# Optimization experiments

Measured on AMD Instinct MI355X. Metric: run time of the kernel, lower is better.

The kernel has to match this reference:

```python
import jax, jax.numpy as jnp
import numpy as np

N = 100000   # nodes
E = 1600000  # edges (node pairs)
D = 64       # msg_feature_len
H = 128      # hidden width of gate/message MLPs


def setup_inputs() -> dict:
    key = jax.random.key(0)
    ks = jax.random.split(key, 10)
    s = 0.05
    return {
        "node_weights": jax.random.uniform(ks[0], (N, 1), dtype=jnp.float32),
        "node_prev_features": jax.random.normal(ks[1], (N, D), dtype=jnp.float32),
        "self_idx": jax.random.randint(ks[2], (E,), 0, N),
        "neighbor_idx": jax.random.randint(ks[3], (E,), 0, N),
        "gw1": jax.random.normal(ks[4], (2 * D, H), dtype=jnp.float32) * s,
        "gb1": jnp.zeros((H,), jnp.float32),
        "gw2": jax.random.normal(ks[5], (H, 1), dtype=jnp.float32) * s,
        "gb2": jnp.zeros((1,), jnp.float32),
        "mw1": jax.random.normal(ks[6], (2 * D, H), dtype=jnp.float32) * s,
        "mb1": jnp.zeros((H,), jnp.float32),
        "mw2": jax.random.normal(ks[7], (H, D), dtype=jnp.float32) * s,
        "mb2": jnp.zeros((D,), jnp.float32),
        "pow_p": jax.random.normal(ks[8], (1,), dtype=jnp.float32),
    }


def reference(node_weights, node_prev_features, self_idx, neighbor_idx,
              gw1, gb1, gw2, gb2, mw1, mb1, mw2, mb2, pow_p):
    # gather + concat: message [E, 2D]
    msg = jnp.concatenate(
        [node_prev_features[self_idx], node_prev_features[neighbor_idx]], axis=1)
    w = node_weights[neighbor_idx]  # [E, 1]

    # gate MLP (Linear -> ReLU -> Linear): [E, 1]
    gate = jax.nn.relu(msg @ gw1 + gb1) @ gw2 + gb2
    # segment-softmax over edges grouped by self_idx, weighted by w**pow
    gmax = jax.ops.segment_max(gate, self_idx, num_segments=N)  # [N, 1]
    gate = (w ** pow_p) * jnp.exp(gate - gmax[self_idx])
    gsum = jax.ops.segment_sum(gate, self_idx, num_segments=N)  # [N, 1]
    gate = gate / (gsum[self_idx] + 1e-10)

    # message MLP: [E, D]
    x = jax.nn.relu(msg @ mw1 + mb1) @ mw2 + mb2

    # weighted scatter-sum back to nodes; single head -> mean is identity
    node_update = jax.ops.segment_sum(gate * x, self_idx, num_segments=N)
    return node_update + node_prev_features
```

## Files before the change

### kernel.cpp

```cpp
#include <hip/hip_runtime.h>
#include <hip/hip_bf16.h>

typedef __bf16 bf16x8 __attribute__((ext_vector_type(8)));
typedef float f32x4 __attribute__((ext_vector_type(4)));
typedef float f32x2 __attribute__((ext_vector_type(2)));

#define WIN 64
#define TILE 112
#define CHUNK 7
#define HSTR 136
#define SCAN_BLK 1024
#define SENT 0x7f7f7f7f

static __device__ __forceinline__ void dec8(unsigned x, unsigned y, float* o) {
    f32x2 a = __builtin_amdgcn_cvt_pk_f32_fp8(x, false);
    f32x2 b = __builtin_amdgcn_cvt_pk_f32_fp8(x, true);
    f32x2 c = __builtin_amdgcn_cvt_pk_f32_fp8(y, false);
    f32x2 d = __builtin_amdgcn_cvt_pk_f32_fp8(y, true);
    o[0] = a[0]; o[1] = a[1]; o[2] = b[0]; o[3] = b[1];
    o[4] = c[0]; o[5] = c[1]; o[6] = d[0]; o[7] = d[1];
}

__global__ void k_wconv(const float* __restrict__ gw1, const float* __restrict__ mw1,
                        const float* __restrict__ mw2,
                        __bf16* __restrict__ Bt, __bf16* __restrict__ mw2t,
                        int* __restrict__ hist, int* __restrict__ s_lo,
                        int* __restrict__ s_hi, int N, int NB)
{
    int i = blockIdx.x * 256 + threadIdx.x;
    if (i < 32768) {
        int c = i >> 6, k = i & 63;
        float v;
        if (c < 128)      v = gw1[k * 128 + c];
        else if (c < 256) v = gw1[(64 + k) * 128 + (c - 128)];
        else if (c < 384) v = mw1[k * 128 + (c - 256)];
        else              v = mw1[(64 + k) * 128 + (c - 384)];
        Bt[i] = (__bf16)v;
    } else if (i < 40960) {
        int j = i - 32768;
        int c = j >> 7, k = j & 127;
        mw2t[j] = (__bf16)mw2[k * 64 + c];
    }
    if (i < N) hist[i] = 0;
    if (i < NB) { s_lo[i] = SENT; s_hi[i] = 0; }
}

__global__ void __launch_bounds__(256, 4)
k_tab(const float* __restrict__ feat, const __bf16* __restrict__ Bt,
      const float* __restrict__ gb1, const float* __restrict__ mb1,
      const int* __restrict__ selfi, int* __restrict__ hist,
      unsigned char* __restrict__ Tp, unsigned char* __restrict__ Tq, int N, int E)
{
    __shared__ unsigned char ldsT[2][16][256];

    for (int e = blockIdx.x * 256 + threadIdx.x; e < E; e += gridDim.x * 256)
        atomicAdd(&hist[selfi[e]], 1);

    const int tid = threadIdx.x;
    const int lane = tid & 63, wv = tid >> 6;
    const int la = lane & 15, kg = lane >> 4;
    const int r0 = blockIdx.x * 16;
    if (r0 >= N) return;

    bf16x8 a[2];
    #pragma unroll
    for (int kk = 0; kk < 2; ++kk) {
        const int rr = min(r0 + la, N - 1);
        const float* src = feat + (size_t)rr * 64 + kk * 32 + kg * 8;
        f32x4 f0 = *reinterpret_cast<const f32x4*>(src);
        f32x4 f1 = *reinterpret_cast<const f32x4*>(src + 4);
        #pragma unroll
        for (int j = 0; j < 4; ++j) { a[kk][j] = (__bf16)f0[j]; a[kk][4 + j] = (__bf16)f1[j]; }
    }
    #pragma unroll
    for (int j = 0; j < 8; ++j) {
        const int c = wv * 128 + j * 16 + la;
        float bias = 0.f;
        if (c < 128) bias = gb1[c];
        else if (c >= 256 && c < 384) bias = mb1[c - 256];
        f32x4 acc = {bias, bias, bias, bias};
        #pragma unroll
        for (int kk = 0; kk < 2; ++kk) {
            bf16x8 bb = *reinterpret_cast<const bf16x8*>(Bt + (size_t)c * 64 + kk * 32 + kg * 8);
            acc = __builtin_amdgcn_mfma_f32_16x16x32_bf16(a[kk], bb, acc, 0, 0, 0);
        }
        int tbl, boff;
        if (c < 128)      { tbl = 0; boff = ((c) >> 3) * 16 + (c & 7); }
        else if (c < 256) { const int q = c - 128; tbl = 1; boff = (q >> 3) * 16 + (q & 7); }
        else if (c < 384) { const int q = c - 256; tbl = 0; boff = (q >> 3) * 16 + 8 + (q & 7); }
        else              { const int q = c - 384; tbl = 1; boff = (q >> 3) * 16 + 8 + (q & 7); }
        #pragma unroll
        for (int i = 0; i < 4; ++i) {
            const int pk = __builtin_amdgcn_cvt_pk_fp8_f32(acc[i], acc[i], 0, false);
            ldsT[tbl][kg * 4 + i][boff] = (unsigned char)(pk & 0xff);
        }
    }
    __syncthreads();
    {
        const int row = tid >> 4, v4 = tid & 15;
        if (r0 + row < N) {
            const uint4* s0p = reinterpret_cast<const uint4*>(&ldsT[0][row][0]);
            const uint4* s1p = reinterpret_cast<const uint4*>(&ldsT[1][row][0]);
            reinterpret_cast<uint4*>(Tp + (size_t)(r0 + row) * 256)[v4] = s0p[v4];
            reinterpret_cast<uint4*>(Tq + (size_t)(r0 + row) * 256)[v4] = s1p[v4];
        }
    }
}

__global__ void k_scan1(const int* __restrict__ hist, int* __restrict__ incl,
                        int* __restrict__ bsum, int N)
{
    __shared__ int sd[SCAN_BLK];
    int i = blockIdx.x * SCAN_BLK + threadIdx.x;
    int v = (i < N) ? hist[i] : 0;
    sd[threadIdx.x] = v;
    __syncthreads();
    for (int off = 1; off < SCAN_BLK; off <<= 1) {
        int t = (threadIdx.x >= off) ? sd[threadIdx.x - off] : 0;
        __syncthreads();
        sd[threadIdx.x] += t;
        __syncthreads();
    }
    if (i < N) incl[i] = sd[threadIdx.x];
    if (threadIdx.x == SCAN_BLK - 1) bsum[blockIdx.x] = sd[SCAN_BLK - 1];
}

__global__ void k_scan23(const int* __restrict__ incl, const int* __restrict__ hist,
                         const int* __restrict__ bsum,
                         int* __restrict__ cursor, int* __restrict__ starts,
                         int* __restrict__ s_lo, int* __restrict__ s_hi,
                         float* __restrict__ lpw, const float* __restrict__ nodew,
                         const float* __restrict__ powp,
                         const float* __restrict__ prev, float* __restrict__ out,
                         int N, int E)
{
    __shared__ int boff_s;
    if (threadIdx.x < 64) {
        int part = 0;
        for (int j = threadIdx.x; j < (int)blockIdx.x; j += 64) part += bsum[j];
        #pragma unroll
        for (int sh = 1; sh < 64; sh <<= 1) part += __shfl_xor(part, sh, 64);
        if (threadIdx.x == 0) boff_s = part;
    }
    __syncthreads();
    int i = blockIdx.x * SCAN_BLK + threadIdx.x;
    if (i >= N) return;
    const int h = hist[i];
    const int v = incl[i] - h + boff_s;
    cursor[i] = v;
    starts[i] = v;
    lpw[i] = powp[0] * __logf(nodew[i]);
    if (h > 0) {
        const int b = v / WIN;
        atomicMin(&s_lo[b], i);
        atomicMax(&s_hi[b], i + 1);
    } else {
        const float* ps = prev + (size_t)i * 64;
        float* po = out + (size_t)i * 64;
        for (int k = 0; k < 64; ++k) po[k] = ps[k];
    }
}

__global__ void k_scatter(const int* __restrict__ selfi, const int* __restrict__ nbri,
                          int* __restrict__ cursor, int* __restrict__ nbr_p, int E)
{
    int e = blockIdx.x * 256 + threadIdx.x;
    if (e >= E) return;
    int s = selfi[e];
    int pos = atomicAdd(&cursor[s], 1);
    nbr_p[pos] = nbri[e];
}

__global__ void __launch_bounds__(256, 5)
k_fused(const unsigned char* __restrict__ Tp, const unsigned char* __restrict__ Tq,
        const int* __restrict__ nbr_p, const int* __restrict__ starts,
        const int* __restrict__ s_lo, const int* __restrict__ s_hi,
        const float* __restrict__ lpw,
        const float* __restrict__ gw2, const float* __restrict__ gb2,
        const __bf16* __restrict__ mw2t, const float* __restrict__ mb2,
        const float* __restrict__ prev, float* __restrict__ out,
        int N, int E)
{
    __shared__ __align__(16) unsigned char hlds8[TILE][HSTR];
    __shared__ float logit_s[TILE];
    __shared__ float ginv_s[WIN];
    __shared__ int st_s[WIN + 1];

    const int b = blockIdx.x;
    const int s0 = s_lo[b];
    if (s0 == SENT) return;
    const int s1 = s_hi[b];
    const int nseg = s1 - s0;
    const int e0 = starts[s0];
    const int e1 = (s1 < N) ? starts[s1] : E;
    int ne = e1 - e0;
    if (ne > TILE) ne = TILE;

    const int tid = threadIdx.x;
    for (int j = tid; j <= nseg; j += 256)
        st_s[j] = (j < nseg) ? starts[s0 + j] : e1;
    __syncthreads();

    const int lane = tid & 63, wv = tid >> 6;
    const int g16 = tid >> 4, il = tid & 15;

    {
        const float b2v = gb2[0];
        float w2f[8];
        {
            f32x4 wa = *reinterpret_cast<const f32x4*>(gw2 + il * 8);
            f32x4 wb = *reinterpret_cast<const f32x4*>(gw2 + il * 8 + 4);
            w2f[0] = wa[0]; w2f[1] = wa[1]; w2f[2] = wa[2]; w2f[3] = wa[3];
            w2f[4] = wb[0]; w2f[5] = wb[1]; w2f[6] = wb[2]; w2f[7] = wb[3];
        }
        const int ck = (ne + 15) >> 4;
        const int rb = g16 * ck;
        const int re = min(rb + ck, ne);
        const int m = re - rb;
        if (m > 0) {
            uint4 qv[CHUNK];
            float lpv[CHUNK];
            #pragma unroll
            for (int j = 0; j < CHUNK; ++j) {
                const int rc = (j < m) ? (rb + j) : (re - 1);
                const int nn = nbr_p[e0 + rc];
                qv[j] = *reinterpret_cast<const uint4*>(Tq + (size_t)nn * 256 + il * 16);
                lpv[j] = lpw[nn];
            }
            int cur;
            {
                int lo = 0, hi = nseg - 1;
                while (lo < hi) {
                    const int mid = (lo + hi + 1) >> 1;
                    if (st_s[mid] <= e0 + rb) lo = mid; else hi = mid - 1;
                }
                cur = lo;
            }
            int curlim = st_s[cur + 1];
            float pgf[8], pmf[8];
            {
                const uint4 tpv = *reinterpret_cast<const uint4*>(Tp + (size_t)(s0 + cur) * 256 + il * 16);
                dec8(tpv.x, tpv.y, pgf);
                dec8(tpv.z, tpv.w, pmf);
            }
            #pragma unroll
            for (int j = 0; j < CHUNK; ++j) {
                if (j < m) {
                    const int r = rb + j;
                    if (e0 + r >= curlim) {
                        do { ++cur; curlim = st_s[cur + 1]; } while (e0 + r >= curlim);
                        const uint4 tpv = *reinterpret_cast<const uint4*>(Tp + (size_t)(s0 + cur) * 256 + il * 16);
                        dec8(tpv.x, tpv.y, pgf);
                        dec8(tpv.z, tpv.w, pmf);
                    }
                    float qgv[8], qmv[8];
                    dec8(qv[j].x, qv[j].y, qgv);
                    dec8(qv[j].z, qv[j].w, qmv);
                    float lg = 0.f;
                    float hm[8];
                    #pragma unroll
                    for (int q = 0; q < 8; ++q) {
                        lg = fmaf(fmaxf(pgf[q] + qgv[q], 0.f), w2f[q], lg);
                        hm[q] = fmaxf(pmf[q] + qmv[q], 0.f);
                    }
                    unsigned d0 = __builtin_amdgcn_cvt_pk_fp8_f32(hm[0], hm[1], 0, false);
                    d0 = __builtin_amdgcn_cvt_pk_fp8_f32(hm[2], hm[3], d0, true);
                    unsigned d1 = __builtin_amdgcn_cvt_pk_fp8_f32(hm[4], hm[5], 0, false);
                    d1 = __builtin_amdgcn_cvt_pk_fp8_f32(hm[6], hm[7], d1, true);
                    *reinterpret_cast<uint2*>(&hlds8[r][il * 8]) = make_uint2(d0, d1);
                    #pragma unroll
                    for (int sh = 1; sh < 16; sh <<= 1)
                        lg += __shfl_xor(lg, sh, 16);
                    if (il == 0) logit_s[r] = lg + b2v + lpv[j];
                }
            }
        }
    }
    __syncthreads();

    const int la = lane & 15, kg = lane >> 4;
    const int row0[2] = {wv * 16, 64 + wv * 16};
    const bool lv[2] = {row0[0] < ne, (wv < 3) && (row0[1] < ne)};

    f32x4 c2[2][4] = {};
    #pragma unroll
    for (int kk = 0; kk < 4; ++kk) {
        const int kboff = kk * 32 + kg * 8;
        bf16x8 a[2];
        #pragma unroll
        for (int m2 = 0; m2 < 2; ++m2)
            if (lv[m2]) {
                const uint2 hw = *reinterpret_cast<const uint2*>(&hlds8[row0[m2] + la][kboff]);
                float t[8];
                dec8(hw.x, hw.y, t);
                #pragma unroll
                for (int q = 0; q < 8; ++q) a[m2][q] = (__bf16)t[q];
            }
        #pragma unroll
        for (int n = 0; n < 4; ++n) {
            bf16x8 bb = *reinterpret_cast<const bf16x8*>(mw2t + (size_t)(n * 16 + la) * 128 + kboff);
            #pragma unroll
            for (int m2 = 0; m2 < 2; ++m2)
                if (lv[m2]) c2[m2][n] = __builtin_amdgcn_mfma_f32_16x16x32_bf16(a[m2], bb, c2[m2][n], 0, 0, 0);
        }
    }

    for (int j = g16; j < nseg; j += 16) {
        int a0 = st_s[j] - e0;
        int a1 = st_s[j + 1] - e0;
        if (a1 > ne) a1 = ne;
        float mx = -3.4e38f;
        for (int idx = a0 + il; idx < a1; idx += 16)
            mx = fmaxf(mx, logit_s[idx]);
        #pragma unroll
        for (int sh = 1; sh < 16; sh <<= 1)
            mx = fmaxf(mx, __shfl_xor(mx, sh, 16));
        float sum = 0.f;
        for (int idx = a0 + il; idx < a1; idx += 16) {
            const float g = __expf(logit_s[idx] - mx);
            logit_s[idx] = g;
            sum += g;
        }
        #pragma unroll
        for (int sh = 1; sh < 16; sh <<= 1)
            sum += __shfl_xor(sum, sh, 16);
        if (il == 0) ginv_s[j] = 1.f / (sum + 1e-10f);
    }
    __syncthreads();

    __bf16 (*xb)[68] = reinterpret_cast<__bf16(*)[68]>(&hlds8[0][0]);
    #pragma unroll
    for (int m2 = 0; m2 < 2; ++m2) {
        if (!lv[m2]) continue;
        #pragma unroll
        for (int n = 0; n < 4; ++n) {
            const float b2v = mb2[n * 16 + la];
            #pragma unroll
            for (int i = 0; i < 4; ++i) {
                const int row = row0[m2] + kg * 4 + i;
                const float v = (row < ne) ? logit_s[row] * (c2[m2][n][i] + b2v) : 0.f;
                xb[row][n * 16 + la] = (__bf16)v;
            }
        }
    }
    __syncthreads();

    for (int j = wv; j < nseg; j += 4) {
        int a0 = st_s[j] - e0;
        int a1 = st_s[j + 1] - e0;
        if (a1 > ne) a1 = ne;
        if (a1 <= a0) continue;
        float sum = 0.f;
        for (int r = a0; r < a1; ++r) sum += (float)xb[r][lane];
        const float gi = ginv_s[j];
        const size_t o = (size_t)(s0 + j) * 64 + lane;
        out[o] = prev[o] + sum * gi;
    }
}

extern "C" void kernel_launch(void* const* d_in, const int* in_sizes, int n_in,
                              void* d_out, int out_size, void* d_ws, size_t ws_size,
                              hipStream_t stream)
{
    const float* node_w = (const float*)d_in[0];
    const float* prev   = (const float*)d_in[1];
    const int*   selfi  = (const int*)d_in[2];
    const int*   nbri   = (const int*)d_in[3];
    const float* gw1 = (const float*)d_in[4];
    const float* gb1 = (const float*)d_in[5];
    const float* gw2 = (const float*)d_in[6];
    const float* gb2 = (const float*)d_in[7];
    const float* mw1 = (const float*)d_in[8];
    const float* mb1 = (const float*)d_in[9];
    const float* mw2 = (const float*)d_in[10];
    const float* mb2 = (const float*)d_in[11];
    const float* powp = (const float*)d_in[12];
    const int N = in_sizes[0];
    const int E = in_sizes[2];
    float* out = (float*)d_out;
    const int NB = (E + WIN - 1) / WIN;

    char* ws = (char*)d_ws;
    size_t off = 0;
    auto alloc = [&](size_t bytes) {
        void* p = ws + off;
        off = (off + bytes + 255) & ~(size_t)255;
        return p;
    };
    unsigned char* Tp    = (unsigned char*)alloc((size_t)N * 256);
    unsigned char* Tq    = (unsigned char*)alloc((size_t)N * 256);
    __bf16* Bt           = (__bf16*)alloc(512 * 64 * 2);
    __bf16* mw2t         = (__bf16*)alloc(64 * 128 * 2);
    int* nbr_p           = (int*)alloc((size_t)E * 4);
    int* hist            = (int*)alloc((size_t)N * 4);
    int* cursor          = (int*)alloc((size_t)N * 4);
    int* starts          = (int*)alloc((size_t)N * 4);
    int* incl            = (int*)alloc((size_t)N * 4);
    float* lpw           = (float*)alloc((size_t)N * 4);
    int* s_lo            = (int*)alloc((size_t)NB * 4);
    int* s_hi            = (int*)alloc((size_t)NB * 4);
    const int nb = (N + SCAN_BLK - 1) / SCAN_BLK;
    int* bsum            = (int*)alloc((size_t)nb * 4);

    int initN = N;
    if (initN < 40960) initN = 40960;
    if (initN < NB) initN = NB;
    k_wconv<<<(initN + 255) / 256, 256, 0, stream>>>(gw1, mw1, mw2, Bt, mw2t,
                                                     hist, s_lo, s_hi, N, NB);
    k_tab<<<(N + 15) / 16, 256, 0, stream>>>(prev, Bt, gb1, mb1, selfi, hist, Tp, Tq, N, E);
    k_scan1<<<nb, SCAN_BLK, 0, stream>>>(hist, incl, bsum, N);
    k_scan23<<<nb, SCAN_BLK, 0, stream>>>(incl, hist, bsum, cursor, starts, s_lo, s_hi,
                                          lpw, node_w, powp, prev, out, N, E);
    k_scatter<<<(E + 255) / 256, 256, 0, stream>>>(selfi, nbri, cursor, nbr_p, E);
    k_fused<<<NB, 256, 0, stream>>>(Tp, Tq, nbr_p, starts, s_lo, s_hi, lpw,
                                    gw2, gb2, mw2t, mb2, prev, out, N, E);
}
```

Baseline: 503.1 us.

## Stage fused-kernel hidden activations in bf16 and use shuffle-based block scan

Hidden message-MLP activations are stored in LDS as bf16 instead of fp8, and the weighted outputs as fp32 instead of bf16. This removes the fp8 encode/decode and bf16 conversions around the second MFMA and the segment reduction, at the cost of doubled LDS footprint and traffic. The block prefix scan now uses wave shuffles instead of a barrier-heavy Hillis-Steele loop. Buffer initialization moves from the weight-conversion kernel to hipMemsetAsync calls, which adds launches.

```diff
diff --git a/kernel.cpp b/kernel.cpp
--- a/kernel.cpp
+++ b/kernel.cpp
@@ -8,7 +8,7 @@
 #define WIN 64
 #define TILE 112
 #define CHUNK 7
-#define HSTR 136
+#define LSTR 136
 #define SCAN_BLK 1024
 #define SENT 0x7f7f7f7f
 
@@ -23,9 +23,7 @@
 
 __global__ void k_wconv(const float* __restrict__ gw1, const float* __restrict__ mw1,
                         const float* __restrict__ mw2,
-                        __bf16* __restrict__ Bt, __bf16* __restrict__ mw2t,
-                        int* __restrict__ hist, int* __restrict__ s_lo,
-                        int* __restrict__ s_hi, int N, int NB)
+                        __bf16* __restrict__ Bt, __bf16* __restrict__ mw2t)
 {
     int i = blockIdx.x * 256 + threadIdx.x;
     if (i < 32768) {
@@ -41,8 +39,6 @@
         int c = j >> 7, k = j & 127;
         mw2t[j] = (__bf16)mw2[k * 64 + c];
     }
-    if (i < N) hist[i] = 0;
-    if (i < NB) { s_lo[i] = SENT; s_hi[i] = 0; }
 }
 
 __global__ void __launch_bounds__(256, 4)
@@ -110,19 +106,30 @@
 __global__ void k_scan1(const int* __restrict__ hist, int* __restrict__ incl,
                         int* __restrict__ bsum, int N)
 {
-    __shared__ int sd[SCAN_BLK];
-    int i = blockIdx.x * SCAN_BLK + threadIdx.x;
-    int v = (i < N) ? hist[i] : 0;
-    sd[threadIdx.x] = v;
-    __syncthreads();
-    for (int off = 1; off < SCAN_BLK; off <<= 1) {
-        int t = (threadIdx.x >= off) ? sd[threadIdx.x - off] : 0;
-        __syncthreads();
-        sd[threadIdx.x] += t;
-        __syncthreads();
-    }
-    if (i < N) incl[i] = sd[threadIdx.x];
-    if (threadIdx.x == SCAN_BLK - 1) bsum[blockIdx.x] = sd[SCAN_BLK - 1];
+    __shared__ int wsum[16];
+    const int i = blockIdx.x * SCAN_BLK + threadIdx.x;
+    const int lane = threadIdx.x & 63, w = threadIdx.x >> 6;
+    int s = (i < N) ? hist[i] : 0;
+    #pragma unroll
+    for (int off = 1; off < 64; off <<= 1) {
+        const int t = __shfl_up(s, off, 64);
+        if (lane >= off) s += t;
+    }
+    if (lane == 63) wsum[w] = s;
+    __syncthreads();
+    if (w == 0) {
+        int ws = (lane < 16) ? wsum[lane] : 0;
+        #pragma unroll
+        for (int off = 1; off < 16; off <<= 1) {
+            const int t = __shfl_up(ws, off, 64);
+            if (lane >= off) ws += t;
+        }
+        if (lane < 16) wsum[lane] = ws;
+    }
+    __syncthreads();
+    if (w > 0) s += wsum[w - 1];
+    if (i < N) incl[i] = s;
+    if (threadIdx.x == SCAN_BLK - 1) bsum[blockIdx.x] = s;
 }
 
 __global__ void k_scan23(const int* __restrict__ incl, const int* __restrict__ hist,
@@ -181,7 +188,7 @@
         const float* __restrict__ prev, float* __restrict__ out,
         int N, int E)
 {
-    __shared__ __align__(16) unsigned char hlds8[TILE][HSTR];
+    __shared__ __align__(16) __bf16 hlds[TILE][LSTR];
     __shared__ float logit_s[TILE];
     __shared__ float ginv_s[WIN];
     __shared__ int st_s[WIN + 1];
@@ -257,17 +264,13 @@
                     dec8(qv[j].x, qv[j].y, qgv);
                     dec8(qv[j].z, qv[j].w, qmv);
                     float lg = 0.f;
-                    float hm[8];
+                    bf16x8 hv;
                     #pragma unroll
                     for (int q = 0; q < 8; ++q) {
                         lg = fmaf(fmaxf(pgf[q] + qgv[q], 0.f), w2f[q], lg);
-                        hm[q] = fmaxf(pmf[q] + qmv[q], 0.f);
+                        hv[q] = (__bf16)fmaxf(pmf[q] + qmv[q], 0.f);
                     }
-                    unsigned d0 = __builtin_amdgcn_cvt_pk_fp8_f32(hm[0], hm[1], 0, false);
-                    d0 = __builtin_amdgcn_cvt_pk_fp8_f32(hm[2], hm[3], d0, true);
-                    unsigned d1 = __builtin_amdgcn_cvt_pk_fp8_f32(hm[4], hm[5], 0, false);
-                    d1 = __builtin_amdgcn_cvt_pk_fp8_f32(hm[6], hm[7], d1, true);
-                    *reinterpret_cast<uint2*>(&hlds8[r][il * 8]) = make_uint2(d0, d1);
+                    *reinterpret_cast<bf16x8*>(&hlds[r][il * 8]) = hv;
                     #pragma unroll
                     for (int sh = 1; sh < 16; sh <<= 1)
                         lg += __shfl_xor(lg, sh, 16);
@@ -285,20 +288,14 @@
     f32x4 c2[2][4] = {};
     #pragma unroll
     for (int kk = 0; kk < 4; ++kk) {
-        const int kboff = kk * 32 + kg * 8;
+        const int kbase = kk * 32 + kg * 8;
         bf16x8 a[2];
         #pragma unroll
         for (int m2 = 0; m2 < 2; ++m2)
-            if (lv[m2]) {
-                const uint2 hw = *reinterpret_cast<const uint2*>(&hlds8[row0[m2] + la][kboff]);
-                float t[8];
-                dec8(hw.x, hw.y, t);
-                #pragma unroll
-                for (int q = 0; q < 8; ++q) a[m2][q] = (__bf16)t[q];
-            }
+            if (lv[m2]) a[m2] = *reinterpret_cast<const bf16x8*>(&hlds[row0[m2] + la][kbase]);
         #pragma unroll
         for (int n = 0; n < 4; ++n) {
-            bf16x8 bb = *reinterpret_cast<const bf16x8*>(mw2t + (size_t)(n * 16 + la) * 128 + kboff);
+            bf16x8 bb = *reinterpret_cast<const bf16x8*>(mw2t + (size_t)(n * 16 + la) * 128 + kbase);
             #pragma unroll
             for (int m2 = 0; m2 < 2; ++m2)
                 if (lv[m2]) c2[m2][n] = __builtin_amdgcn_mfma_f32_16x16x32_bf16(a[m2], bb, c2[m2][n], 0, 0, 0);
@@ -328,19 +325,22 @@
     }
     __syncthreads();
 
-    __bf16 (*xb)[68] = reinterpret_cast<__bf16(*)[68]>(&hlds8[0][0]);
+    float (*xb)[68] = reinterpret_cast<float(*)[68]>(&hlds[0][0]);
     #pragma unroll
     for (int m2 = 0; m2 < 2; ++m2) {
         if (!lv[m2]) continue;
+        float cf[4];
+        #pragma unroll
+        for (int i = 0; i < 4; ++i) {
+            const int row = row0[m2] + kg * 4 + i;
+            cf[i] = (row < ne) ? logit_s[row] : 0.f;
+        }
         #pragma unroll
         for (int n = 0; n < 4; ++n) {
             const float b2v = mb2[n * 16 + la];
             #pragma unroll
-            for (int i = 0; i < 4; ++i) {
-                const int row = row0[m2] + kg * 4 + i;
-                const float v = (row < ne) ? logit_s[row] * (c2[m2][n][i] + b2v) : 0.f;
-                xb[row][n * 16 + la] = (__bf16)v;
-            }
+            for (int i = 0; i < 4; ++i)
+                xb[row0[m2] + kg * 4 + i][n * 16 + la] = cf[i] * (c2[m2][n][i] + b2v);
         }
     }
     __syncthreads();
@@ -351,7 +351,7 @@
         if (a1 > ne) a1 = ne;
         if (a1 <= a0) continue;
         float sum = 0.f;
-        for (int r = a0; r < a1; ++r) sum += (float)xb[r][lane];
+        for (int r = a0; r < a1; ++r) sum += xb[r][lane];
         const float gi = ginv_s[j];
         const size_t o = (size_t)(s0 + j) * 64 + lane;
         out[o] = prev[o] + sum * gi;
@@ -402,11 +402,10 @@
     const int nb = (N + SCAN_BLK - 1) / SCAN_BLK;
     int* bsum            = (int*)alloc((size_t)nb * 4);
 
-    int initN = N;
-    if (initN < 40960) initN = 40960;
-    if (initN < NB) initN = NB;
-    k_wconv<<<(initN + 255) / 256, 256, 0, stream>>>(gw1, mw1, mw2, Bt, mw2t,
-                                                     hist, s_lo, s_hi, N, NB);
+    k_wconv<<<160, 256, 0, stream>>>(gw1, mw1, mw2, Bt, mw2t);
+    hipMemsetAsync(hist, 0, (size_t)N * 4, stream);
+    hipMemsetAsync(s_lo, 0x7f, (size_t)NB * 4, stream);
+    hipMemsetAsync(s_hi, 0, (size_t)NB * 4, stream);
     k_tab<<<(N + 15) / 16, 256, 0, stream>>>(prev, Bt, gb1, mb1, selfi, hist, Tp, Tq, N, E);
     k_scan1<<<nb, SCAN_BLK, 0, stream>>>(hist, incl, bsum, N);
     k_scan23<<<nb, SCAN_BLK, 0, stream>>>(incl, hist, bsum, cursor, starts, s_lo, s_hi,
```

Result: no change. 498.9 us (-0.8%).
